# Kernel tuning notes

Measured on AMD Instinct MI355X. Metric: run time of the kernel, lower is better.

The kernel has to match this reference:

```python
import jax, jax.numpy as jnp
import numpy as np

B, CIN, COUT, H, W = 8, 64, 64, 96, 96
K = 3
PAD = 1
BN_EPS = 1e-5


def conv2d(x, w, b):
    # plain 3x3 conv, stride 1, pad 1 (NCHW / OIHW)
    y = jax.lax.conv_general_dilated(
        x, w, window_strides=(1, 1), padding=[(PAD, PAD), (PAD, PAD)],
        dimension_numbers=("NCHW", "OIHW", "NCHW"))
    return y + b[None, :, None, None]


def setup_inputs() -> dict:
    key = jax.random.key(0)
    ks = jax.random.split(key, 6)
    s = 0.05  # small init so offsets stay near the regular grid (matches DCN zero-ish init)
    return {
        "x": jax.random.normal(ks[0], (B, CIN, H, W), jnp.float32),
        "offset_w": jax.random.normal(ks[1], (2 * K * K, CIN, K, K), jnp.float32) * s,
        "offset_b": jnp.zeros((2 * K * K,), jnp.float32),
        "mod_w": jax.random.normal(ks[2], (K * K, CIN, K, K), jnp.float32) * s,
        "mod_b": jnp.zeros((K * K,), jnp.float32),
        "weight": jax.random.normal(ks[3], (COUT, CIN, K, K), jnp.float32) * s,
        "bias": jax.random.normal(ks[4], (COUT,), jnp.float32) * s,
        "bn_gamma": jnp.ones((COUT,), jnp.float32),
        "bn_beta": jnp.zeros((COUT,), jnp.float32),
        "bn_mean": jnp.zeros((COUT,), jnp.float32),
        "bn_var": jnp.ones((COUT,), jnp.float32),
    }


def _deform_sample(xb, py, px):
    # xb: [C,H,W]; py, px: [K2,H,W] fractional sampling coords (zero outside image)
    y0 = jnp.floor(py)
    x0 = jnp.floor(px)
    dy = py - y0
    dx = px - x0

    def gather(yi, xi):
        valid = ((yi >= 0) & (yi < H) & (xi >= 0) & (xi < W)).astype(xb.dtype)
        yc = jnp.clip(yi, 0, H - 1).astype(jnp.int32)
        xc = jnp.clip(xi, 0, W - 1).astype(jnp.int32)
        return xb[:, yc, xc] * valid  # [C,K2,H,W]

    v00 = gather(y0, x0)
    v01 = gather(y0, x0 + 1.0)
    v10 = gather(y0 + 1.0, x0)
    v11 = gather(y0 + 1.0, x0 + 1.0)
    return (v00 * (1 - dy) * (1 - dx) + v01 * (1 - dy) * dx
            + v10 * dy * (1 - dx) + v11 * dy * dx)  # [C,K2,H,W]


def reference(x, offset_w, offset_b, mod_w, mod_b, weight, bias,
              bn_gamma, bn_beta, bn_mean, bn_var):
    # 1) predict offsets and modulation mask (DCNv2)
    offset = conv2d(x, offset_w, offset_b)                 # [B, 2*K2, H, W]
    modulator = 2.0 * jax.nn.sigmoid(conv2d(x, mod_w, mod_b))  # [B, K2, H, W]

    off = offset.reshape(B, K * K, 2, H, W)
    off_y, off_x = off[:, :, 0], off[:, :, 1]              # [B,K2,H,W]

    # 2) base sampling grid per kernel tap
    ky, kx = jnp.meshgrid(jnp.arange(K), jnp.arange(K), indexing="ij")
    base_y = (jnp.arange(H)[None, :, None] - PAD
              + ky.reshape(-1)[:, None, None]).astype(jnp.float32)  # [K2,H,1]
    base_x = (jnp.arange(W)[None, None, :] - PAD
              + kx.reshape(-1)[:, None, None]).astype(jnp.float32)  # [K2,1,W]
    py = base_y + off_y                                    # [B,K2,H,W]
    px = base_x + off_x

    # 3) bilinear gather at irregular positions, modulate per tap
    sampled = jax.vmap(_deform_sample)(x, py, px)          # [B,C,K2,H,W]
    sampled = sampled * modulator[:, None]                 # broadcast over C

    # 4) contract taps with the regular conv weight
    wk = weight.reshape(COUT, CIN, K * K)
    y = jnp.einsum("bckhw,ock->bohw", sampled, wk) + bias[None, :, None, None]

    # 5) BatchNorm (inference: running stats) + ReLU
    inv = bn_gamma / jnp.sqrt(bn_var + BN_EPS)
    y = (y - bn_mean[None, :, None, None]) * inv[None, :, None, None] \
        + bn_beta[None, :, None, None]
    return jax.nn.relu(y)
```

## Files before the change

kernel.cpp:

```cpp
#include <hip/hip_runtime.h>
#include <hip/hip_bf16.h>
#include <hip/hip_fp16.h>
#include <math.h>

#define BB 8
#define HH 96
#define WW 96
#define HW 9216
#define BN_EPS 1e-5f

typedef _Float16 f16x2 __attribute__((ext_vector_type(2)));
typedef _Float16 f16x8 __attribute__((ext_vector_type(8)));
typedef float f32x4 __attribute__((ext_vector_type(4)));

union HU  { _Float16 h; unsigned short u; };
union UH2 { unsigned u; f16x2 h; };
union U4H { uint4 u; f16x2 h2[4]; };

#define OFF_W4   0
#define SZ_W4    (BB*9*HW*16)
#define OFF_XT   (OFF_W4 + SZ_W4)
#define SZ_XT    (BB*HW*64*2)
#define OFF_XY   (OFF_XT + SZ_XT)
#define SZ_XY    (BB*9*HW*4)
#define OFF_WB   (OFF_XY + SZ_XY)
#define SZ_WB    (64*576*2)
#define OFF_WO   (OFF_WB + SZ_WB)
#define SZ_WO    (32*576*2)
#define OFF_BN   (OFF_WO + SZ_WO)
#define SZ_BN    (64*2*4)

__global__ __launch_bounds__(256) void prep_kernel(
    const float* __restrict__ weight, const float* __restrict__ offw,
    const float* __restrict__ modw,
    const float* __restrict__ bias, const float* __restrict__ gamma,
    const float* __restrict__ beta, const float* __restrict__ mean,
    const float* __restrict__ var,
    _Float16* __restrict__ wB, _Float16* __restrict__ wOff,
    float* __restrict__ bnS, float* __restrict__ bnB) {
  int tid = blockIdx.x * 256 + threadIdx.x;
  if (tid < 64 * 576) {
    int o = tid / 576, ck = tid % 576;
    int k = ck >> 6, c = ck & 63;
    wB[tid] = (_Float16)weight[o * 576 + c * 9 + k];
  }
  int t2 = tid - 64 * 576;
  if (t2 >= 0 && t2 < 32 * 576) {
    int oc = t2 / 576, kcol = t2 % 576;
    int kk = kcol >> 6, c = kcol & 63;
    float v = 0.f;
    if (oc < 18)      v = offw[(oc * 64 + c) * 9 + kk];
    else if (oc < 27) v = modw[((oc - 18) * 64 + c) * 9 + kk];
    wOff[t2] = (_Float16)v;
  }
  int t3 = tid - (64 * 576 + 32 * 576);
  if (t3 >= 0 && t3 < 64) {
    float inv = gamma[t3] * rsqrtf(var[t3] + BN_EPS);
    bnS[t3] = inv;
    bnB[t3] = (bias[t3] - mean[t3]) * inv + beta[t3];
  }
}

__global__ __launch_bounds__(256) void transpose_x_kernel(
    const float* __restrict__ x, _Float16* __restrict__ xT) {
  __shared__ float tile[64][65];
  int tid = threadIdx.x;
  int b = blockIdx.x & 7;
  int hwb = (blockIdx.x >> 3) * 64;
  int col = tid & 63, g = tid >> 6;
  float r[16];
#pragma unroll
  for (int it = 0; it < 16; ++it)
    r[it] = x[(b * 64 + it * 4 + g) * HW + hwb + col];
  __builtin_amdgcn_sched_barrier(0);
#pragma unroll
  for (int it = 0; it < 16; ++it)
    tile[it * 4 + g][col] = r[it];
  __syncthreads();
#pragma unroll
  for (int it = 0; it < 16; ++it) {
    int p = it * 4 + g;
    xT[(size_t)(b * HW + hwb + p) * 64 + col] = (_Float16)tile[col][p];
  }
}

__device__ __forceinline__ unsigned rep16(float w) {
  HU cv; cv.h = (_Float16)w;
  return 0x10001u * (unsigned)cv.u;
}

__global__ __launch_bounds__(256, 8) void conv_offsets_kernel(
    const _Float16* __restrict__ xTh, const _Float16* __restrict__ wOff,
    const float* __restrict__ offb, const float* __restrict__ modb,
    uint4* __restrict__ w4, unsigned* __restrict__ xy) {
  __shared__ __attribute__((aligned(16))) _Float16 sN[3 * 34 * 70];
  __shared__ float o_off[32 * 33];

  int tid = threadIdx.x;
  int lane = tid & 63;
  int wv = __builtin_amdgcn_readfirstlane(tid >> 6);

  int bi = blockIdx.x;
  int b = bi & 7, rem = bi >> 3;
  int h = rem / 3, w0 = (rem % 3) * 32;

  const _Float16* xb = xTh + (size_t)b * HW * 64;
  _Float16 sv[26];
#pragma unroll
  for (int i = 0; i < 26; ++i) {
    int p = wv + 4 * i;
    _Float16 v = (_Float16)0.f;
    if (p < 102) {
      int row = p / 34, col = p - row * 34;
      int y = h + row - 1, xx = w0 + col - 1;
      if ((y >= 0) && (y < HH) && (xx >= 0) && (xx < WW))
        v = xb[(size_t)(y * WW + xx) * 64 + lane];
    }
    sv[i] = v;
  }
  __builtin_amdgcn_sched_barrier(0);
#pragma unroll
  for (int i = 0; i < 26; ++i) {
    int p = wv + 4 * i;
    if (p < 102) {
      int row = p / 34, col = p - row * 34;
      sN[(row * 34 + col) * 70 + lane] = sv[i];
    }
  }
  __syncthreads();

  int r = lane & 15, g = lane >> 4;
  int mt = wv >> 1, nt = wv & 1;
  int px = mt * 16 + r;
  const _Float16* bp = wOff + (nt * 16 + r) * 576 + g * 8;
  f32x4 acc = {0.f, 0.f, 0.f, 0.f};
#pragma unroll
  for (int s = 0; s < 18; ++s) {
    int kk = s >> 1, ky = kk / 3, kx = kk - ky * 3;
    f16x8 a = *(const f16x8*)&sN[(ky * 34 + px + kx) * 70 + (s & 1) * 32 + g * 8];
    f16x8 bb = *(const f16x8*)(bp + s * 32);
    acc = __builtin_amdgcn_mfma_f32_16x16x32_f16(a, bb, acc, 0, 0, 0);
  }
#pragma unroll
  for (int j = 0; j < 4; ++j)
    o_off[(mt * 16 + g * 4 + j) * 33 + nt * 16 + r] = acc[j];
  __syncthreads();

  for (int it = tid; it < 288; it += 256) {
    int pxx = it & 31, k = it >> 5;
    int ky = k / 3, kx = k - ky * 3;
    int w = w0 + pxx;

    float offy = o_off[pxx * 33 + 2 * k]     + offb[2 * k];
    float offx = o_off[pxx * 33 + 2 * k + 1] + offb[2 * k + 1];
    float mod  = 2.f / (1.f + __expf(-(o_off[pxx * 33 + 18 + k] + modb[k])));

    float py  = (float)(h - 1 + ky) + offy;
    float px_ = (float)(w - 1 + kx) + offx;
    float y0f = floorf(py), x0f = floorf(px_);
    float dy = py - y0f, dx = px_ - x0f;
    int y0 = (int)y0f, x0 = (int)x0f;
    int y1 = y0 + 1, x1 = x0 + 1;
    bool vy0 = (y0 >= 0) && (y0 < HH), vy1 = (y1 >= 0) && (y1 < HH);
    bool vx0 = (x0 >= 0) && (x0 < WW), vx1 = (x1 >= 0) && (x1 < WW);
    float w00 = (vy0 && vx0) ? (1.f - dy) * (1.f - dx) * mod : 0.f;
    float w01 = (vy0 && vx1) ? (1.f - dy) * dx * mod : 0.f;
    float w10 = (vy1 && vx0) ? dy * (1.f - dx) * mod : 0.f;
    float w11 = (vy1 && vx1) ? dy * dx * mod : 0.f;
    int y0c = min(max(y0, 0), HH - 1), y1c = min(max(y1, 0), HH - 1);
    int x0c = min(max(x0, 0), WW - 1), x1c = min(max(x1, 0), WW - 1);
    unsigned pk = (unsigned)y0c | ((unsigned)y1c << 8) |
                  ((unsigned)x0c << 16) | ((unsigned)x1c << 24);
    int idx = (b * 9 + k) * HW + h * WW + w;
    w4[idx] = make_uint4(rep16(w00), rep16(w01), rep16(w10), rep16(w11));
    xy[idx] = pk;
  }
}

__global__ __launch_bounds__(256, 8) void dcn_main_kernel(
    const _Float16* __restrict__ xT,
    const uint4* __restrict__ w4pk, const unsigned* __restrict__ xy,
    const _Float16* __restrict__ wB,
    const float* __restrict__ bnS, const float* __restrict__ bnB,
    float* __restrict__ out) {
  __shared__ __attribute__((aligned(16))) _Float16 s_A[16 * 584];
  float* o_lds = (float*)s_A;

  int tid = threadIdx.x;
  int lane = tid & 63;
  int wv = __builtin_amdgcn_readfirstlane(tid >> 6);

  int bi = blockIdx.x;
  int b = bi & 7, t = bi >> 3;
  int h = t / 6, w0 = (t - (t / 6) * 6) * 16;
  int hwrow = h * WW + w0;

  const unsigned char* xbc = (const unsigned char*)(xT + (size_t)b * HW * 64);

  int hsel = lane >> 5;
  unsigned ch4 = (unsigned)((lane & 31) << 2);

#pragma unroll
  for (int px = 0; px < 4; ++px) {
    int pl = wv * 4 + px;
    int hw = hwrow + pl;
    unsigned q[9];
    uint4 wq[9];
#pragma unroll
    for (int k = 0; k < 9; ++k) {
      q[k]  = xy[(b * 9 + k) * HW + hw];
      wq[k] = w4pk[(b * 9 + k) * HW + hw];
    }

#pragma unroll
    for (int p4 = 0; p4 < 4; ++p4) {
      const int kA = 2 * p4;
      unsigned qa = q[kA], qb = q[kA + 1];
      unsigned aY0 = qa & 255u, aY1 = (qa >> 8) & 255u;
      unsigned aX0 = (qa >> 16) & 255u, aX1 = qa >> 24;
      unsigned bY0 = qb & 255u, bY1 = (qb >> 8) & 255u;
      unsigned bX0 = (qb >> 16) & 255u, bX1 = qb >> 24;
      unsigned oA0 = (aY0 * WW + aX0) << 7, oA1 = (aY0 * WW + aX1) << 7;
      unsigned oA2 = (aY1 * WW + aX0) << 7, oA3 = (aY1 * WW + aX1) << 7;
      unsigned oB0 = (bY0 * WW + bX0) << 7, oB1 = (bY0 * WW + bX1) << 7;
      unsigned oB2 = (bY1 * WW + bX0) << 7, oB3 = (bY1 * WW + bX1) << 7;
      unsigned a0 = (hsel ? oB0 : oA0) + ch4;
      unsigned a1 = (hsel ? oB1 : oA1) + ch4;
      unsigned a2 = (hsel ? oB2 : oA2) + ch4;
      unsigned a3 = (hsel ? oB3 : oA3) + ch4;
      unsigned t0 = *(const unsigned*)(xbc + a0);
      unsigned t1 = *(const unsigned*)(xbc + a1);
      unsigned t2 = *(const unsigned*)(xbc + a2);
      unsigned t3 = *(const unsigned*)(xbc + a3);
      U4H Wa, Wb;
      Wa.u = wq[kA]; Wb.u = wq[kA + 1];
      f16x2 W0 = hsel ? Wb.h2[0] : Wa.h2[0];
      f16x2 W1 = hsel ? Wb.h2[1] : Wa.h2[1];
      f16x2 W2 = hsel ? Wb.h2[2] : Wa.h2[2];
      f16x2 W3 = hsel ? Wb.h2[3] : Wa.h2[3];
      UH2 v0, v1, v2, v3, s;
      v0.u = t0; v1.u = t1; v2.u = t2; v3.u = t3;
      s.h = v0.h * W0 + v1.h * W1 + v2.h * W2 + v3.h * W3;
      *(unsigned*)&s_A[pl * 584 + (kA + hsel) * 64 + (int)(ch4 >> 1)] = s.u;
    }
    {
      unsigned qa = q[8];
      unsigned aY0 = qa & 255u, aY1 = (qa >> 8) & 255u;
      unsigned aX0 = (qa >> 16) & 255u, aX1 = qa >> 24;
      unsigned a0 = (((aY0 * WW + aX0) << 7)) + ch4;
      unsigned a1 = (((aY0 * WW + aX1) << 7)) + ch4;
      unsigned a2 = (((aY1 * WW + aX0) << 7)) + ch4;
      unsigned a3 = (((aY1 * WW + aX1) << 7)) + ch4;
      unsigned t0 = *(const unsigned*)(xbc + a0);
      unsigned t1 = *(const unsigned*)(xbc + a1);
      unsigned t2 = *(const unsigned*)(xbc + a2);
      unsigned t3 = *(const unsigned*)(xbc + a3);
      U4H W; W.u = wq[8];
      UH2 v0, v1, v2, v3, s;
      v0.u = t0; v1.u = t1; v2.u = t2; v3.u = t3;
      s.h = v0.h * W.h2[0] + v1.h * W.h2[1] + v2.h * W.h2[2] + v3.h * W.h2[3];
      if (lane < 32)
        *(unsigned*)&s_A[pl * 584 + 512 + (int)(ch4 >> 1)] = s.u;
    }
  }
  __syncthreads();

  int r = lane & 15, g = lane >> 4;
  const _Float16* arow = s_A + r * 584 + g * 8;
  const _Float16* bp = wB + (wv * 16 + r) * 576 + g * 8;
  f32x4 accA = {0.f, 0.f, 0.f, 0.f}, accB = {0.f, 0.f, 0.f, 0.f};
#pragma unroll 3
  for (int s = 0; s < 18; s += 2) {
    f16x8 a0 = *(const f16x8*)(arow + s * 32);
    f16x8 b0 = *(const f16x8*)(bp + s * 32);
    f16x8 a1 = *(const f16x8*)(arow + s * 32 + 32);
    f16x8 b1 = *(const f16x8*)(bp + s * 32 + 32);
    accA = __builtin_amdgcn_mfma_f32_16x16x32_f16(a0, b0, accA, 0, 0, 0);
    accB = __builtin_amdgcn_mfma_f32_16x16x32_f16(a1, b1, accB, 0, 0, 0);
  }

  int o = wv * 16 + r;
  float sc = bnS[o], sh = bnB[o];
  __syncthreads();
#pragma unroll
  for (int j = 0; j < 4; ++j) {
    int px = g * 4 + j;
    o_lds[o * 20 + px] = fmaxf((accA[j] + accB[j]) * sc + sh, 0.f);
  }
  __syncthreads();

  int oo = tid >> 2, q = tid & 3;
  float4 u = *(const float4*)&o_lds[oo * 20 + q * 4];
  *(float4*)(out + (size_t)(b * 64 + oo) * HW + hwrow + q * 4) = u;
}

extern "C" void kernel_launch(void* const* d_in, const int* in_sizes, int n_in,
                              void* d_out, int out_size, void* d_ws, size_t ws_size,
                              hipStream_t stream) {
  const float* x      = (const float*)d_in[0];
  const float* offw   = (const float*)d_in[1];
  const float* offb   = (const float*)d_in[2];
  const float* modw   = (const float*)d_in[3];
  const float* modb   = (const float*)d_in[4];
  const float* weight = (const float*)d_in[5];
  const float* bias   = (const float*)d_in[6];
  const float* gamma  = (const float*)d_in[7];
  const float* beta   = (const float*)d_in[8];
  const float* mean   = (const float*)d_in[9];
  const float* var    = (const float*)d_in[10];

  char* ws = (char*)d_ws;
  uint4*     w4    = (uint4*)(ws + OFF_W4);
  _Float16*  xTh   = (_Float16*)(ws + OFF_XT);
  unsigned*  xybuf = (unsigned*)(ws + OFF_XY);
  _Float16*  wB    = (_Float16*)(ws + OFF_WB);
  _Float16*  wOff  = (_Float16*)(ws + OFF_WO);
  float*     bnS   = (float*)(ws + OFF_BN);
  float*     bnB   = bnS + 64;

  prep_kernel<<<217, 256, 0, stream>>>(weight, offw, modw, bias, gamma, beta,
                                       mean, var, wB, wOff, bnS, bnB);
  transpose_x_kernel<<<1152, 256, 0, stream>>>(x, xTh);
  conv_offsets_kernel<<<2304, 256, 0, stream>>>(xTh, wOff, offb, modb, w4, xybuf);
  dcn_main_kernel<<<4608, 256, 0, stream>>>(xTh, w4, xybuf, wB, bnS, bnB,
                                            (float*)d_out);
}
```

Baseline: 101.1 us.

## Stage local input window in LDS for deformable bilinear gathers

```diff
diff --git a/kernel.cpp b/kernel.cpp
--- a/kernel.cpp
+++ b/kernel.cpp
@@ -8,6 +8,8 @@
 #define WW 96
 #define HW 9216
 #define BN_EPS 1e-5f
+#define WR 14
+#define WC 32
 
 typedef _Float16 f16x2 __attribute__((ext_vector_type(2)));
 typedef _Float16 f16x8 __attribute__((ext_vector_type(8)));
@@ -16,6 +18,9 @@
 union HU  { _Float16 h; unsigned short u; };
 union UH2 { unsigned u; f16x2 h; };
 union U4H { uint4 u; f16x2 h2[4]; };
+
+typedef const __attribute__((address_space(1))) unsigned char g1_t;
+typedef __attribute__((address_space(3))) unsigned char l3_t;
 
 #define OFF_W4   0
 #define SZ_W4    (BB*9*HW*16)
@@ -177,13 +182,14 @@
   }
 }
 
-__global__ __launch_bounds__(256, 8) void dcn_main_kernel(
+__global__ __launch_bounds__(256, 2) void dcn_main_kernel(
     const _Float16* __restrict__ xT,
     const uint4* __restrict__ w4pk, const unsigned* __restrict__ xy,
     const _Float16* __restrict__ wB,
     const float* __restrict__ bnS, const float* __restrict__ bnB,
     float* __restrict__ out) {
   __shared__ __attribute__((aligned(16))) _Float16 s_A[16 * 584];
+  __shared__ __attribute__((aligned(16))) _Float16 s_win[WR * WC * 64];
   float* o_lds = (float*)s_A;
 
   int tid = threadIdx.x;
@@ -197,8 +203,25 @@
 
   const unsigned char* xbc = (const unsigned char*)(xT + (size_t)b * HW * 64);
 
+  int y0w = h - 6;  y0w = y0w < 0 ? 0 : (y0w > HH - WR ? HH - WR : y0w);
+  int x0w = w0 - 8; x0w = x0w < 0 ? 0 : (x0w > WW - WC ? WW - WC : x0w);
+  int yHi = y0w + WR - 1, xHi = x0w + WC - 1;
+
+#pragma unroll
+  for (int i = 0; i < 14; ++i) {
+    int j = wv + 4 * i;
+    int row = j >> 2, seg = j & 3;
+    unsigned srcOff = (unsigned)((((y0w + row) * WW + x0w) << 7) + seg * 1024);
+    __builtin_amdgcn_global_load_lds(
+        (g1_t*)(xbc + srcOff + (unsigned)(lane << 4)),
+        (l3_t*)s_win + j * 1024, 16, 0, 0);
+  }
+  asm volatile("s_waitcnt vmcnt(0)" ::: "memory");
+  __syncthreads();
+
   int hsel = lane >> 5;
   unsigned ch4 = (unsigned)((lane & 31) << 2);
+  const char* wp = (const char*)s_win;
 
 #pragma unroll
   for (int px = 0; px < 4; ++px) {
@@ -216,22 +239,34 @@
     for (int p4 = 0; p4 < 4; ++p4) {
       const int kA = 2 * p4;
       unsigned qa = q[kA], qb = q[kA + 1];
-      unsigned aY0 = qa & 255u, aY1 = (qa >> 8) & 255u;
-      unsigned aX0 = (qa >> 16) & 255u, aX1 = qa >> 24;
-      unsigned bY0 = qb & 255u, bY1 = (qb >> 8) & 255u;
-      unsigned bX0 = (qb >> 16) & 255u, bX1 = qb >> 24;
-      unsigned oA0 = (aY0 * WW + aX0) << 7, oA1 = (aY0 * WW + aX1) << 7;
-      unsigned oA2 = (aY1 * WW + aX0) << 7, oA3 = (aY1 * WW + aX1) << 7;
-      unsigned oB0 = (bY0 * WW + bX0) << 7, oB1 = (bY0 * WW + bX1) << 7;
-      unsigned oB2 = (bY1 * WW + bX0) << 7, oB3 = (bY1 * WW + bX1) << 7;
-      unsigned a0 = (hsel ? oB0 : oA0) + ch4;
-      unsigned a1 = (hsel ? oB1 : oA1) + ch4;
-      unsigned a2 = (hsel ? oB2 : oA2) + ch4;
-      unsigned a3 = (hsel ? oB3 : oA3) + ch4;
-      unsigned t0 = *(const unsigned*)(xbc + a0);
-      unsigned t1 = *(const unsigned*)(xbc + a1);
-      unsigned t2 = *(const unsigned*)(xbc + a2);
-      unsigned t3 = *(const unsigned*)(xbc + a3);
+      int aY0 = qa & 255, aY1 = (qa >> 8) & 255, aX0 = (qa >> 16) & 255, aX1 = qa >> 24;
+      int bY0 = qb & 255, bY1 = (qb >> 8) & 255, bX0 = (qb >> 16) & 255, bX1 = qb >> 24;
+      unsigned t0, t1, t2, t3;
+      bool inw = aY0 >= y0w && aY1 <= yHi && aX0 >= x0w && aX1 <= xHi &&
+                 bY0 >= y0w && bY1 <= yHi && bX0 >= x0w && bX1 <= xHi;
+      if (inw) {
+        unsigned rA0 = (unsigned)((((aY0 - y0w) << 5) + (aX0 - x0w)) << 7);
+        unsigned rA1 = (unsigned)((((aY0 - y0w) << 5) + (aX1 - x0w)) << 7);
+        unsigned rA2 = (unsigned)((((aY1 - y0w) << 5) + (aX0 - x0w)) << 7);
+        unsigned rA3 = (unsigned)((((aY1 - y0w) << 5) + (aX1 - x0w)) << 7);
+        unsigned rB0 = (unsigned)((((bY0 - y0w) << 5) + (bX0 - x0w)) << 7);
+        unsigned rB1 = (unsigned)((((bY0 - y0w) << 5) + (bX1 - x0w)) << 7);
+        unsigned rB2 = (unsigned)((((bY1 - y0w) << 5) + (bX0 - x0w)) << 7);
+        unsigned rB3 = (unsigned)((((bY1 - y0w) << 5) + (bX1 - x0w)) << 7);
+        t0 = *(const unsigned*)(wp + ((hsel ? rB0 : rA0) + ch4));
+        t1 = *(const unsigned*)(wp + ((hsel ? rB1 : rA1) + ch4));
+        t2 = *(const unsigned*)(wp + ((hsel ? rB2 : rA2) + ch4));
+        t3 = *(const unsigned*)(wp + ((hsel ? rB3 : rA3) + ch4));
+      } else {
+        unsigned oA0 = (unsigned)((aY0 * WW + aX0) << 7), oA1 = (unsigned)((aY0 * WW + aX1) << 7);
+        unsigned oA2 = (unsigned)((aY1 * WW + aX0) << 7), oA3 = (unsigned)((aY1 * WW + aX1) << 7);
+        unsigned oB0 = (unsigned)((bY0 * WW + bX0) << 7), oB1 = (unsigned)((bY0 * WW + bX1) << 7);
+        unsigned oB2 = (unsigned)((bY1 * WW + bX0) << 7), oB3 = (unsigned)((bY1 * WW + bX1) << 7);
+        t0 = *(const unsigned*)(xbc + ((hsel ? oB0 : oA0) + ch4));
+        t1 = *(const unsigned*)(xbc + ((hsel ? oB1 : oA1) + ch4));
+        t2 = *(const unsigned*)(xbc + ((hsel ? oB2 : oA2) + ch4));
+        t3 = *(const unsigned*)(xbc + ((hsel ? oB3 : oA3) + ch4));
+      }
       U4H Wa, Wb;
       Wa.u = wq[kA]; Wb.u = wq[kA + 1];
       f16x2 W0 = hsel ? Wb.h2[0] : Wa.h2[0];
@@ -245,16 +280,26 @@
     }
     {
       unsigned qa = q[8];
-      unsigned aY0 = qa & 255u, aY1 = (qa >> 8) & 255u;
-      unsigned aX0 = (qa >> 16) & 255u, aX1 = qa >> 24;
-      unsigned a0 = (((aY0 * WW + aX0) << 7)) + ch4;
-      unsigned a1 = (((aY0 * WW + aX1) << 7)) + ch4;
-      unsigned a2 = (((aY1 * WW + aX0) << 7)) + ch4;
-      unsigned a3 = (((aY1 * WW + aX1) << 7)) + ch4;
-      unsigned t0 = *(const unsigned*)(xbc + a0);
-      unsigned t1 = *(const unsigned*)(xbc + a1);
-      unsigned t2 = *(const unsigned*)(xbc + a2);
-      unsigned t3 = *(const unsigned*)(xbc + a3);
+      int aY0 = qa & 255, aY1 = (qa >> 8) & 255, aX0 = (qa >> 16) & 255, aX1 = qa >> 24;
+      unsigned t0, t1, t2, t3;
+      bool inw = aY0 >= y0w && aY1 <= yHi && aX0 >= x0w && aX1 <= xHi;
+      if (inw) {
+        unsigned r0 = (unsigned)((((aY0 - y0w) << 5) + (aX0 - x0w)) << 7);
+        unsigned r1 = (unsigned)((((aY0 - y0w) << 5) + (aX1 - x0w)) << 7);
+        unsigned r2 = (unsigned)((((aY1 - y0w) << 5) + (aX0 - x0w)) << 7);
+        unsigned r3 = (unsigned)((((aY1 - y0w) << 5) + (aX1 - x0w)) << 7);
+        t0 = *(const unsigned*)(wp + (r0 + ch4));
+        t1 = *(const unsigned*)(wp + (r1 + ch4));
+        t2 = *(const unsigned*)(wp + (r2 + ch4));
+        t3 = *(const unsigned*)(wp + (r3 + ch4));
+      } else {
+        unsigned o0 = (unsigned)((aY0 * WW + aX0) << 7), o1 = (unsigned)((aY0 * WW + aX1) << 7);
+        unsigned o2 = (unsigned)((aY1 * WW + aX0) << 7), o3 = (unsigned)((aY1 * WW + aX1) << 7);
+        t0 = *(const unsigned*)(xbc + (o0 + ch4));
+        t1 = *(const unsigned*)(xbc + (o1 + ch4));
+        t2 = *(const unsigned*)(xbc + (o2 + ch4));
+        t3 = *(const unsigned*)(xbc + (o3 + ch4));
+      }
       U4H W; W.u = wq[8];
       UH2 v0, v1, v2, v3, s;
       v0.u = t0; v1.u = t1; v2.u = t2; v3.u = t3;
```

Measured after the change: 136.0 us. 1.34x slower.

## Fuse offset/modulator conv into main deformable conv kernel via shared LDS

Applied to the files above, without the earlier changes.

```diff
diff --git a/kernel.cpp b/kernel.cpp
--- a/kernel.cpp
+++ b/kernel.cpp
@@ -17,13 +17,9 @@
 union UH2 { unsigned u; f16x2 h; };
 union U4H { uint4 u; f16x2 h2[4]; };
 
-#define OFF_W4   0
-#define SZ_W4    (BB*9*HW*16)
-#define OFF_XT   (OFF_W4 + SZ_W4)
+#define OFF_XT   0
 #define SZ_XT    (BB*HW*64*2)
-#define OFF_XY   (OFF_XT + SZ_XT)
-#define SZ_XY    (BB*9*HW*4)
-#define OFF_WB   (OFF_XY + SZ_XY)
+#define OFF_WB   (OFF_XT + SZ_XT)
 #define SZ_WB    (64*576*2)
 #define OFF_WO   (OFF_WB + SZ_WB)
 #define SZ_WO    (32*576*2)
@@ -89,29 +85,39 @@
   return 0x10001u * (unsigned)cv.u;
 }
 
-__global__ __launch_bounds__(256, 8) void conv_offsets_kernel(
-    const _Float16* __restrict__ xTh, const _Float16* __restrict__ wOff,
+__global__ __launch_bounds__(256, 6) void dcn_fused_kernel(
+    const _Float16* __restrict__ xT, const _Float16* __restrict__ wOff,
     const float* __restrict__ offb, const float* __restrict__ modb,
-    uint4* __restrict__ w4, unsigned* __restrict__ xy) {
-  __shared__ __attribute__((aligned(16))) _Float16 sN[3 * 34 * 70];
-  __shared__ float o_off[32 * 33];
+    const _Float16* __restrict__ wB,
+    const float* __restrict__ bnS, const float* __restrict__ bnB,
+    float* __restrict__ out) {
+  __shared__ __attribute__((aligned(16))) char uLDS[18688];
+  __shared__ unsigned xys[144];
+  __shared__ __attribute__((aligned(16))) uint4 w4s[144];
+  _Float16* sN     = (_Float16*)uLDS;
+  float*    o_part = (float*)(uLDS + 7776);
+  _Float16* s_A    = (_Float16*)uLDS;
+  float*    o_lds  = (float*)uLDS;
 
   int tid = threadIdx.x;
   int lane = tid & 63;
   int wv = __builtin_amdgcn_readfirstlane(tid >> 6);
 
   int bi = blockIdx.x;
-  int b = bi & 7, rem = bi >> 3;
-  int h = rem / 3, w0 = (rem % 3) * 32;
-
-  const _Float16* xb = xTh + (size_t)b * HW * 64;
-  _Float16 sv[26];
-#pragma unroll
-  for (int i = 0; i < 26; ++i) {
+  int b = bi & 7, t = bi >> 3;
+  int h = t / 6, w0 = (t - (t / 6) * 6) * 16;
+  int hwrow = h * WW + w0;
+
+  const _Float16* xb = xT + (size_t)b * HW * 64;
+  const unsigned char* xbc = (const unsigned char*)xb;
+
+  _Float16 sv[14];
+#pragma unroll
+  for (int i = 0; i < 14; ++i) {
     int p = wv + 4 * i;
     _Float16 v = (_Float16)0.f;
-    if (p < 102) {
-      int row = p / 34, col = p - row * 34;
+    if (p < 54) {
+      int row = p / 18, col = p - row * 18;
       int y = h + row - 1, xx = w0 + col - 1;
       if ((y >= 0) && (y < HH) && (xx >= 0) && (xx < WW))
         v = xb[(size_t)(y * WW + xx) * 64 + lane];
@@ -120,40 +126,39 @@
   }
   __builtin_amdgcn_sched_barrier(0);
 #pragma unroll
-  for (int i = 0; i < 26; ++i) {
+  for (int i = 0; i < 14; ++i) {
     int p = wv + 4 * i;
-    if (p < 102) {
-      int row = p / 34, col = p - row * 34;
-      sN[(row * 34 + col) * 70 + lane] = sv[i];
+    if (p < 54) sN[p * 72 + lane] = sv[i];
+  }
+  __syncthreads();
+
+  int r = lane & 15, g = lane >> 4;
+  {
+    int nt = wv & 1, ks = wv >> 1;
+    const _Float16* bp = wOff + (nt * 16 + r) * 576 + ks * 288 + g * 8;
+    f32x4 acc = {0.f, 0.f, 0.f, 0.f};
+#pragma unroll
+    for (int si = 0; si < 9; ++si) {
+      int s = ks * 9 + si;
+      int kk = s >> 1, ky = kk / 3, kx = kk - ky * 3, ch = s & 1;
+      f16x8 a  = *(const f16x8*)&sN[(ky * 18 + r + kx) * 72 + ch * 32 + g * 8];
+      f16x8 bb = *(const f16x8*)(bp + si * 32);
+      acc = __builtin_amdgcn_mfma_f32_16x16x32_f16(a, bb, acc, 0, 0, 0);
     }
-  }
-  __syncthreads();
-
-  int r = lane & 15, g = lane >> 4;
-  int mt = wv >> 1, nt = wv & 1;
-  int px = mt * 16 + r;
-  const _Float16* bp = wOff + (nt * 16 + r) * 576 + g * 8;
-  f32x4 acc = {0.f, 0.f, 0.f, 0.f};
-#pragma unroll
-  for (int s = 0; s < 18; ++s) {
-    int kk = s >> 1, ky = kk / 3, kx = kk - ky * 3;
-    f16x8 a = *(const f16x8*)&sN[(ky * 34 + px + kx) * 70 + (s & 1) * 32 + g * 8];
-    f16x8 bb = *(const f16x8*)(bp + s * 32);
-    acc = __builtin_amdgcn_mfma_f32_16x16x32_f16(a, bb, acc, 0, 0, 0);
-  }
-#pragma unroll
-  for (int j = 0; j < 4; ++j)
-    o_off[(mt * 16 + g * 4 + j) * 33 + nt * 16 + r] = acc[j];
-  __syncthreads();
-
-  for (int it = tid; it < 288; it += 256) {
-    int pxx = it & 31, k = it >> 5;
+#pragma unroll
+    for (int j = 0; j < 4; ++j)
+      o_part[ks * 528 + (g * 4 + j) * 33 + nt * 16 + r] = acc[j];
+  }
+  __syncthreads();
+
+  if (tid < 144) {
+    int px = tid / 9, k = tid - px * 9;
     int ky = k / 3, kx = k - ky * 3;
-    int w = w0 + pxx;
-
-    float offy = o_off[pxx * 33 + 2 * k]     + offb[2 * k];
-    float offx = o_off[pxx * 33 + 2 * k + 1] + offb[2 * k + 1];
-    float mod  = 2.f / (1.f + __expf(-(o_off[pxx * 33 + 18 + k] + modb[k])));
+    int w = w0 + px;
+    float offy = o_part[px * 33 + 2 * k]     + o_part[528 + px * 33 + 2 * k]     + offb[2 * k];
+    float offx = o_part[px * 33 + 2 * k + 1] + o_part[528 + px * 33 + 2 * k + 1] + offb[2 * k + 1];
+    float mz   = o_part[px * 33 + 18 + k]    + o_part[528 + px * 33 + 18 + k]    + modb[k];
+    float mod  = 2.f / (1.f + __expf(-mz));
 
     float py  = (float)(h - 1 + ky) + offy;
     float px_ = (float)(w - 1 + kx) + offx;
@@ -169,33 +174,11 @@
     float w11 = (vy1 && vx1) ? dy * dx * mod : 0.f;
     int y0c = min(max(y0, 0), HH - 1), y1c = min(max(y1, 0), HH - 1);
     int x0c = min(max(x0, 0), WW - 1), x1c = min(max(x1, 0), WW - 1);
-    unsigned pk = (unsigned)y0c | ((unsigned)y1c << 8) |
-                  ((unsigned)x0c << 16) | ((unsigned)x1c << 24);
-    int idx = (b * 9 + k) * HW + h * WW + w;
-    w4[idx] = make_uint4(rep16(w00), rep16(w01), rep16(w10), rep16(w11));
-    xy[idx] = pk;
-  }
-}
-
-__global__ __launch_bounds__(256, 8) void dcn_main_kernel(
-    const _Float16* __restrict__ xT,
-    const uint4* __restrict__ w4pk, const unsigned* __restrict__ xy,
-    const _Float16* __restrict__ wB,
-    const float* __restrict__ bnS, const float* __restrict__ bnB,
-    float* __restrict__ out) {
-  __shared__ __attribute__((aligned(16))) _Float16 s_A[16 * 584];
-  float* o_lds = (float*)s_A;
-
-  int tid = threadIdx.x;
-  int lane = tid & 63;
-  int wv = __builtin_amdgcn_readfirstlane(tid >> 6);
-
-  int bi = blockIdx.x;
-  int b = bi & 7, t = bi >> 3;
-  int h = t / 6, w0 = (t - (t / 6) * 6) * 16;
-  int hwrow = h * WW + w0;
-
-  const unsigned char* xbc = (const unsigned char*)(xT + (size_t)b * HW * 64);
+    xys[tid] = (unsigned)y0c | ((unsigned)y1c << 8) |
+               ((unsigned)x0c << 16) | ((unsigned)x1c << 24);
+    w4s[tid] = make_uint4(rep16(w00), rep16(w01), rep16(w10), rep16(w11));
+  }
+  __syncthreads();
 
   int hsel = lane >> 5;
   unsigned ch4 = (unsigned)((lane & 31) << 2);
@@ -203,14 +186,10 @@
 #pragma unroll
   for (int px = 0; px < 4; ++px) {
     int pl = wv * 4 + px;
-    int hw = hwrow + pl;
+    int mi = pl * 9;
     unsigned q[9];
-    uint4 wq[9];
-#pragma unroll
-    for (int k = 0; k < 9; ++k) {
-      q[k]  = xy[(b * 9 + k) * HW + hw];
-      wq[k] = w4pk[(b * 9 + k) * HW + hw];
-    }
+#pragma unroll
+    for (int k = 0; k < 9; ++k) q[k] = xys[mi + k];
 
 #pragma unroll
     for (int p4 = 0; p4 < 4; ++p4) {
@@ -233,7 +212,7 @@
       unsigned t2 = *(const unsigned*)(xbc + a2);
       unsigned t3 = *(const unsigned*)(xbc + a3);
       U4H Wa, Wb;
-      Wa.u = wq[kA]; Wb.u = wq[kA + 1];
+      Wa.u = w4s[mi + kA]; Wb.u = w4s[mi + kA + 1];
       f16x2 W0 = hsel ? Wb.h2[0] : Wa.h2[0];
       f16x2 W1 = hsel ? Wb.h2[1] : Wa.h2[1];
       f16x2 W2 = hsel ? Wb.h2[2] : Wa.h2[2];
@@ -255,7 +234,7 @@
       unsigned t1 = *(const unsigned*)(xbc + a1);
       unsigned t2 = *(const unsigned*)(xbc + a2);
       unsigned t3 = *(const unsigned*)(xbc + a3);
-      U4H W; W.u = wq[8];
+      U4H W; W.u = w4s[mi + 8];
       UH2 v0, v1, v2, v3, s;
       v0.u = t0; v1.u = t1; v2.u = t2; v3.u = t3;
       s.h = v0.h * W.h2[0] + v1.h * W.h2[1] + v2.h * W.h2[2] + v3.h * W.h2[3];
@@ -265,7 +244,6 @@
   }
   __syncthreads();
 
-  int r = lane & 15, g = lane >> 4;
   const _Float16* arow = s_A + r * 584 + g * 8;
   const _Float16* bp = wB + (wv * 16 + r) * 576 + g * 8;
   f32x4 accA = {0.f, 0.f, 0.f, 0.f}, accB = {0.f, 0.f, 0.f, 0.f};
@@ -289,9 +267,9 @@
   }
   __syncthreads();
 
-  int oo = tid >> 2, q = tid & 3;
-  float4 u = *(const float4*)&o_lds[oo * 20 + q * 4];
-  *(float4*)(out + (size_t)(b * 64 + oo) * HW + hwrow + q * 4) = u;
+  int oo = tid >> 2, qd = tid & 3;
+  float4 u = *(const float4*)&o_lds[oo * 20 + qd * 4];
+  *(float4*)(out + (size_t)(b * 64 + oo) * HW + hwrow + qd * 4) = u;
 }
 
 extern "C" void kernel_launch(void* const* d_in, const int* in_sizes, int n_in,
@@ -310,9 +288,7 @@
   const float* var    = (const float*)d_in[10];
 
   char* ws = (char*)d_ws;
-  uint4*     w4    = (uint4*)(ws + OFF_W4);
   _Float16*  xTh   = (_Float16*)(ws + OFF_XT);
-  unsigned*  xybuf = (unsigned*)(ws + OFF_XY);
   _Float16*  wB    = (_Float16*)(ws + OFF_WB);
   _Float16*  wOff  = (_Float16*)(ws + OFF_WO);
   float*     bnS   = (float*)(ws + OFF_BN);
@@ -321,7 +297,6 @@
   prep_kernel<<<217, 256, 0, stream>>>(weight, offw, modw, bias, gamma, beta,
                                        mean, var, wB, wOff, bnS, bnB);
   transpose_x_kernel<<<1152, 256, 0, stream>>>(x, xTh);
-  conv_offsets_kernel<<<2304, 256, 0, stream>>>(xTh, wOff, offb, modb, w4, xybuf);
-  dcn_main_kernel<<<4608, 256, 0, stream>>>(xTh, w4, xybuf, wB, bnS, bnB,
-                                            (float*)d_out);
-}
+  dcn_fused_kernel<<<4608, 256, 0, stream>>>(xTh, wOff, offb, modb, wB,
+                                             bnS, bnB, (float*)d_out);
+}
```

After: 89.66 us, median of 2. 1.13x faster.
